# Performance work log

Hardware: AMD Instinct MI355X
Metric: run time of the kernel (lower is better)

## Reference

```python
import jax, jax.numpy as jnp
import numpy as np

H = 1024
B = 8
S = 2048

def setup_inputs() -> dict:
    key = jax.random.key(0)
    ks = jax.random.split(key, 16)
    w = lambda k, shp: (jax.random.normal(k, shp, dtype=jnp.float32) * 0.02)
    return {
        "hidden_states": jax.random.normal(ks[0], (B, S, H), dtype=jnp.float32),
        "context_vector": jax.random.normal(ks[1], (B, H), dtype=jnp.float32),
        # nn.Linear weights stored torch-style as [out, in]
        "Wq": w(ks[2], (H, H)), "bq": w(ks[3], (H,)),
        "Wk": w(ks[4], (H, H)), "bk": w(ks[5], (H,)),
        "Wv": w(ks[6], (H, H)), "bv": w(ks[7], (H,)),
        "Wcq": w(ks[8], (H, H)),  # only .weight.t() used in original (no bias)
        "Wck": w(ks[9], (H, H)),
        "g_qh": jax.random.normal(ks[10], (H, 1), dtype=jnp.float32),
        "g_kh": jax.random.normal(ks[11], (H, 1), dtype=jnp.float32),
        "g_qc": jax.random.normal(ks[12], (H, 1), dtype=jnp.float32),
        "g_kc": jax.random.normal(ks[13], (H, 1), dtype=jnp.float32),
    }

def reference(hidden_states, context_vector, Wq, bq, Wk, bk, Wv, bv, Wcq, Wck, g_qh, g_kh, g_qc, g_kc):
    # Linear projections (torch Linear: x @ W.T + b)
    query = jnp.einsum('bsh,oh->bso', hidden_states, Wq) + bq   # [B,S,H]
    key_  = jnp.einsum('bsh,oh->bso', hidden_states, Wk) + bk
    value = jnp.einsum('bsh,oh->bso', hidden_states, Wv) + bv

    # gate = sigmoid(Q @ g_h + (ctx @ g_c)[:,None,:])  -> [B,S,1]
    q_gate = jax.nn.sigmoid(query @ g_qh + (context_vector @ g_qc)[:, None, :])
    k_gate = jax.nn.sigmoid(key_  @ g_kh + (context_vector @ g_kc)[:, None, :])

    # context projections: ctx @ weight.t() (no bias in original usage) -> [B,1,H]
    ctx_q = (context_vector @ Wcq.T)[:, None, :]
    ctx_k = (context_vector @ Wck.T)[:, None, :]

    query_hat = (1.0 - q_gate) * query + q_gate * ctx_q
    key_hat   = (1.0 - k_gate) * key_  + k_gate * ctx_k

    scale = 1.0 / jnp.sqrt(jnp.asarray(H, dtype=jnp.float32))
    scores = jnp.einsum('bqh,bkh->bqk', query_hat, key_hat) * scale  # [B,S,S]
    probs = jax.nn.softmax(scores, axis=-1)
    output = jnp.einsum('bqk,bkh->bqh', probs, value)  # [B,S,H]
    return (output, scores)
```

## Files before the change

### kernel.cpp

```cpp
#include <hip/hip_runtime.h>
#include <cstdint>
#include <cstddef>

#define H 1024
#define NB 8
#define S 2048
#define MROWS (NB*S)

using short8 = __attribute__((ext_vector_type(8))) short;
using f32x4  = __attribute__((ext_vector_type(4))) float;

__device__ __forceinline__ unsigned short f2bf(float f){
  union { float f; unsigned int u; } c; c.f = f;
  unsigned int u = c.u;
  return (unsigned short)((u + 0x7fffu + ((u >> 16) & 1u)) >> 16);
}


__global__ void k_cvt3(const float* __restrict__ a, const float* __restrict__ b, const float* __restrict__ c,
                       unsigned short* __restrict__ oa, unsigned short* __restrict__ ob, unsigned short* __restrict__ oc){
  const float* src = blockIdx.y == 0 ? a : (blockIdx.y == 1 ? b : c);
  unsigned short* dst = blockIdx.y == 0 ? oa : (blockIdx.y == 1 ? ob : oc);
  int i = (blockIdx.x * 256 + threadIdx.x) * 4;
  float4 v = *reinterpret_cast<const float4*>(src + i);
  ushort4 o;
  o.x = f2bf(v.x); o.y = f2bf(v.y); o.z = f2bf(v.z); o.w = f2bf(v.w);
  *reinterpret_cast<ushort4*>(dst + i) = o;
}

__global__ void k_colproj(const float* __restrict__ Wq_, const float* __restrict__ gq_,
                          const float* __restrict__ Wk_, const float* __restrict__ gk_,
                          float* __restrict__ up){
  const float* W = blockIdx.z ? Wk_ : Wq_;
  const float* g = blockIdx.z ? gk_ : gq_;
  const int in = blockIdx.x * 256 + threadIdx.x;
  const int o0 = blockIdx.y * 128;
  float s = 0.f;
  for (int o = 0; o < 128; ++o) s = fmaf(W[(size_t)(o0 + o) * H + in], g[o0 + o], s);
  up[(blockIdx.z * 8 + blockIdx.y) * 1024 + in] = s;
}

__global__ void k_ucombine(const float* __restrict__ up, float* __restrict__ uq, float* __restrict__ uk){
  int i = blockIdx.x * 256 + threadIdx.x;
  int m = i >> 10, j = i & 1023;
  float s = 0.f;
  #pragma unroll
  for (int c = 0; c < 8; ++c) s += up[(m * 8 + c) * 1024 + j];
  (m ? uk : uq)[j] = s;
}

__global__ __launch_bounds__(256) void k_ctxproj(const float* __restrict__ Wcq, const float* __restrict__ Wck,
    const float* __restrict__ ctx, float* __restrict__ outq, float* __restrict__ outk){
  __shared__ float cs[NB * H];
  const float* W = blockIdx.y ? Wck : Wcq;
  float* out = blockIdx.y ? outk : outq;
  const int t = threadIdx.x;
  for (int i = t; i < NB * H; i += 256) cs[i] = ctx[i];
  __syncthreads();
  const int wid = t >> 6, lane = t & 63;
  const int row = blockIdx.x * 4 + wid;
  float a[NB];
  #pragma unroll
  for (int b = 0; b < NB; ++b) a[b] = 0.f;
  for (int i0 = 0; i0 < H; i0 += 64){
    const float w = W[(size_t)row * H + i0 + lane];
    #pragma unroll
    for (int b = 0; b < NB; ++b) a[b] = fmaf(w, cs[b * H + i0 + lane], a[b]);
  }
  #pragma unroll
  for (int b = 0; b < NB; ++b){
    float v = a[b];
    #pragma unroll
    for (int off = 32; off > 0; off >>= 1) v += __shfl_xor(v, off);
    if (lane == 0) out[b * H + row] = v;
  }
}

__device__ float block_dot(const float* a, const float* b, float* red, int t){
  float s = 0.f;
  for (int i = t; i < H; i += 256) s = fmaf(a[i], b[i], s);
  red[t] = s;
  __syncthreads();
  for (int off = 128; off > 0; off >>= 1){
    if (t < off) red[t] += red[t + off];
    __syncthreads();
  }
  float r = red[0];
  __syncthreads();
  return r;
}

__global__ void k_scalars(const float* __restrict__ bq, const float* __restrict__ gqh,
                          const float* __restrict__ bk, const float* __restrict__ gkh,
                          const float* __restrict__ ctx, const float* __restrict__ gqc,
                          const float* __restrict__ gkc, float* __restrict__ scal){
  __shared__ float red[256];
  const int t = threadIdx.x;
  float v;
  v = block_dot(bq, gqh, red, t); if (t == 0) scal[0] = v;
  v = block_dot(bk, gkh, red, t); if (t == 0) scal[1] = v;
  for (int b = 0; b < NB; ++b){
    v = block_dot(ctx + b * H, gqc, red, t); if (t == 0) scal[2 + b] = v;
    v = block_dot(ctx + b * H, gkc, red, t); if (t == 0) scal[10 + b] = v;
  }
}

__global__ __launch_bounds__(256) void k_prepass(const float* __restrict__ hs,
    const float* __restrict__ u_q, const float* __restrict__ u_k, const float* __restrict__ scal,
    unsigned short* __restrict__ hsb, float* __restrict__ gq, float* __restrict__ gk){
  const int t = threadIdx.x, wid = t >> 6, lane = t & 63;
  const int row = blockIdx.x * 4 + wid;
  const float* hrow = hs + (size_t)row * H;
  unsigned short* orow = hsb + (size_t)row * H;
  float sq = 0.f, sk = 0.f;
  #pragma unroll
  for (int c = 0; c < 4; ++c){
    const int idx = (lane + c * 64) * 4;
    float4 v  = *reinterpret_cast<const float4*>(hrow + idx);
    float4 uq = *reinterpret_cast<const float4*>(u_q + idx);
    float4 uk = *reinterpret_cast<const float4*>(u_k + idx);
    ushort4 o; o.x = f2bf(v.x); o.y = f2bf(v.y); o.z = f2bf(v.z); o.w = f2bf(v.w);
    *reinterpret_cast<ushort4*>(orow + idx) = o;
    sq += v.x*uq.x + v.y*uq.y + v.z*uq.z + v.w*uq.w;
    sk += v.x*uk.x + v.y*uk.y + v.z*uk.z + v.w*uk.w;
  }
  #pragma unroll
  for (int off = 32; off > 0; off >>= 1){
    sq += __shfl_xor(sq, off);
    sk += __shfl_xor(sk, off);
  }
  if (lane == 0){
    const int b = row >> 11;
    gq[row] = 1.f / (1.f + __expf(-(sq + scal[0] + scal[2 + b])));
    gk[row] = 1.f / (1.f + __expf(-(sk + scal[1] + scal[10 + b])));
  }
}


#define STG(bufi, opi, halfi, koff, P0, P1) \
  { __builtin_amdgcn_global_load_lds((const __attribute__((address_space(1))) void*)(P0 + (koff)), \
      (__attribute__((address_space(3))) void*)((char*)(&lds[bufi][opi][halfi][0]) + (wid*2+0)*1024), 16, 0, 0); \
    __builtin_amdgcn_global_load_lds((const __attribute__((address_space(1))) void*)(P1 + (koff)), \
      (__attribute__((address_space(3))) void*)((char*)(&lds[bufi][opi][halfi][0]) + (wid*2+1)*1024), 16, 0, 0); }
#define STG_A(bufi, halfi, koff) STG(bufi, 0, halfi, koff, sA0, sA1)
#define STG_B(bufi, halfi, koff) STG(bufi, 1, halfi, koff, sB0, sB1)

#define DS_A(bufi, ks, mh) \
  { _Pragma("unroll") for (int m_ = 0; m_ < 4; ++m_){ \
      const int ar_ = wr*128 + ((mh)*4 + m_)*16 + (lane & 15); \
      const int sl_ = (lane >> 4) ^ ((ar_ >> 1) & 3); \
      af[m_] = *reinterpret_cast<const short8*>(&lds[bufi][0][ks][ar_*32 + sl_*8]); } }
#define DS_B(bufi, ks) \
  { _Pragma("unroll") for (int n_ = 0; n_ < 4; ++n_){ \
      const int br_ = wc*64 + n_*16 + (lane & 15); \
      const int sl_ = (lane >> 4) ^ ((br_ >> 1) & 3); \
      bf[n_] = *reinterpret_cast<const short8*>(&lds[bufi][1][ks][br_*32 + sl_*8]); } }
#define MFMA16(mh) \
  { __builtin_amdgcn_s_setprio(1); \
    _Pragma("unroll") for (int m_ = 0; m_ < 4; ++m_) \
      _Pragma("unroll") for (int n_ = 0; n_ < 4; ++n_) \
        acc[(mh)*4 + m_][n_] = __builtin_amdgcn_mfma_f32_16x16x32_bf16(af[m_], bf[n_], acc[(mh)*4 + m_][n_], 0, 0, 0); \
    __builtin_amdgcn_s_setprio(0); }
#define VM4() asm volatile("s_waitcnt vmcnt(4)" ::: "memory");
#define VM0() asm volatile("s_waitcnt vmcnt(0)" ::: "memory");
#define BAR() { asm volatile("" ::: "memory"); __builtin_amdgcn_s_barrier(); asm volatile("" ::: "memory"); }

template<int MODE>
__global__ __launch_bounds__(512, 2)
void k_gemm(const unsigned short* __restrict__ A, const unsigned short* __restrict__ B,
            int K, int ldA, int ldB, long long Abatch, long long Bbatch,
            const float* __restrict__ gate, const float* __restrict__ bias,
            const float* __restrict__ ctxv,
            unsigned short* __restrict__ outb, float* __restrict__ outf,
            long long outBatch, float scale)
{
  __shared__ __align__(16) short lds[2][2][2][8192];

  const int t = threadIdx.x;
  const int wid = t >> 6, lane = t & 63;
  const int wr = wid >> 2, wc = wid & 3;
  const int bz = blockIdx.z;
  const unsigned short* Ab = A + (size_t)bz * (size_t)Abatch;
  const unsigned short* Bb = B + (size_t)bz * (size_t)Bbatch;
  const int row0 = blockIdx.x * 256;
  const int col0 = blockIdx.y * 256;

  const int c0 = (wid*2 + 0)*64 + lane;
  const int c1 = (wid*2 + 1)*64 + lane;
  const int r0s = c0 >> 2, r1s = c1 >> 2;
  const int kc0 = (c0 & 3) ^ ((r0s >> 1) & 3);
  const int kc1 = (c1 & 3) ^ ((r1s >> 1) & 3);
  const unsigned short* sA0 = Ab + (size_t)(row0 + r0s) * (size_t)ldA + kc0*8;
  const unsigned short* sA1 = Ab + (size_t)(row0 + r1s) * (size_t)ldA + kc1*8;
  const unsigned short* sB0 = Bb + (size_t)(col0 + r0s) * (size_t)ldB + kc0*8;
  const unsigned short* sB1 = Bb + (size_t)(col0 + r1s) * (size_t)ldB + kc1*8;

  f32x4 acc[8][4] = {};
  short8 af[4], bf[4];

  STG_A(0, 0, 0); STG_B(0, 0, 0); STG_A(0, 1, 32); STG_B(0, 1, 32);
  VM0(); BAR();

  const int niter = K >> 7;
  for (int it = 0; it < niter; ++it){
    const int t1k = (it*2 + 1) << 6;
    const int t2k = (it*2 + 2) << 6;
    const bool more = (it + 1 < niter);
    DS_A(0, 0, 0); DS_B(0, 0); STG_A(1, 0, t1k); MFMA16(0); BAR();
    DS_A(0, 0, 1); STG_B(1, 0, t1k); MFMA16(1); VM4(); BAR();
    DS_A(0, 1, 0); DS_B(0, 1); STG_A(1, 1, t1k + 32); MFMA16(0); BAR();
    DS_A(0, 1, 1); STG_B(1, 1, t1k + 32); MFMA16(1);
    if (more) { VM4(); } else { VM0(); }
    BAR();
    DS_A(1, 0, 0); DS_B(1, 0); if (more) STG_A(0, 0, t2k); MFMA16(0); BAR();
    DS_A(1, 0, 1); if (more) { STG_B(0, 0, t2k); } MFMA16(1); if (more) VM4(); BAR();
    DS_A(1, 1, 0); DS_B(1, 1); if (more) STG_A(0, 1, t2k + 32); MFMA16(0); BAR();
    DS_A(1, 1, 1); if (more) { STG_B(0, 1, t2k + 32); } MFMA16(1); if (more) VM4(); BAR();
  }

  if constexpr (MODE == 0 || MODE == 1){
    const int b = row0 >> 11;
    #pragma unroll
    for (int mi = 0; mi < 8; ++mi)
      #pragma unroll
      for (int n = 0; n < 4; ++n)
        #pragma unroll
        for (int r = 0; r < 4; ++r){
          const int grow = row0 + wr*128 + mi*16 + (lane >> 4)*4 + r;
          const int gcol = col0 + wc*64 + n*16 + (lane & 15);
          const float g = gate[grow];
          const float q = acc[mi][n][r] + bias[gcol];
          outb[(size_t)grow * H + gcol] = f2bf((1.f - g) * q + g * ctxv[b * H + gcol]);
        }
  } else if constexpr (MODE == 2){
    short* tp = (short*)lds;
    const int bb = row0 >> 11;
    const int s0 = row0 & (S - 1);
    #pragma unroll
    for (int ci = 0; ci < 2; ++ci)
      #pragma unroll
      for (int cj = 0; cj < 2; ++cj){
        __syncthreads();
        if (wr == ci && (wc >> 1) == cj){
          const int lc0 = (wc & 1) * 64;
          #pragma unroll
          for (int mi = 0; mi < 8; ++mi)
            #pragma unroll
            for (int n = 0; n < 4; ++n)
              #pragma unroll
              for (int r = 0; r < 4; ++r){
                const int lr = mi*16 + (lane >> 4)*4 + r;
                const int lc = lc0 + n*16 + (lane & 15);
                tp[lr*129 + lc] = (short)f2bf(acc[mi][n][r] + bias[col0 + cj*128 + lc]);
              }
        }
        __syncthreads();
        const int hl = t >> 2;
        const int sb = (t & 3) * 32;
        unsigned short* vout = outb + (size_t)bb * H * S + (size_t)(col0 + cj*128 + hl) * S
                                    + (size_t)(s0 + ci*128 + sb);
        #pragma unroll
        for (int i2 = 0; i2 < 32; i2 += 4){
          ushort4 o;
          o.x = (unsigned short)tp[(sb + i2 + 0)*129 + hl];
          o.y = (unsigned short)tp[(sb + i2 + 1)*129 + hl];
          o.z = (unsigned short)tp[(sb + i2 + 2)*129 + hl];
          o.w = (unsigned short)tp[(sb + i2 + 3)*129 + hl];
          *reinterpret_cast<ushort4*>(vout + i2) = o;
        }
      }
  } else if constexpr (MODE == 3){
    #pragma unroll
    for (int mi = 0; mi < 8; ++mi)
      #pragma unroll
      for (int n = 0; n < 4; ++n)
        #pragma unroll
        for (int r = 0; r < 4; ++r){
          const int grow = row0 + wr*128 + mi*16 + (lane >> 4)*4 + r;
          const int gcol = col0 + wc*64 + n*16 + (lane & 15);
          outf[(size_t)bz * (size_t)outBatch + (size_t)grow * S + gcol] = acc[mi][n][r] * scale;
        }
  } else {
    #pragma unroll
    for (int mi = 0; mi < 8; ++mi)
      #pragma unroll
      for (int n = 0; n < 4; ++n)
        #pragma unroll
        for (int r = 0; r < 4; ++r){
          const int grow = row0 + wr*128 + mi*16 + (lane >> 4)*4 + r;
          const int gcol = col0 + wc*64 + n*16 + (lane & 15);
          outf[(size_t)bz * (size_t)outBatch + (size_t)grow * H + gcol] = acc[mi][n][r];
        }
  }
}

__global__ __launch_bounds__(256) void k_softmax(const float* __restrict__ scores,
                                                 unsigned short* __restrict__ probs){
  const int row = blockIdx.x;
  const float* srow = scores + (size_t)row * S;
  unsigned short* prow = probs + (size_t)row * S;
  const int t = threadIdx.x, wid = t >> 6, lane = t & 63;
  __shared__ float red[8];
  float4 v0 = *reinterpret_cast<const float4*>(srow + t * 4);
  float4 v1 = *reinterpret_cast<const float4*>(srow + 1024 + t * 4);
  float m = fmaxf(fmaxf(fmaxf(v0.x, v0.y), fmaxf(v0.z, v0.w)),
                  fmaxf(fmaxf(v1.x, v1.y), fmaxf(v1.z, v1.w)));
  #pragma unroll
  for (int off = 32; off > 0; off >>= 1) m = fmaxf(m, __shfl_xor(m, off));
  if (lane == 0) red[wid] = m;
  __syncthreads();
  m = fmaxf(fmaxf(red[0], red[1]), fmaxf(red[2], red[3]));
  float4 e0, e1;
  e0.x = __expf(v0.x - m); e0.y = __expf(v0.y - m); e0.z = __expf(v0.z - m); e0.w = __expf(v0.w - m);
  e1.x = __expf(v1.x - m); e1.y = __expf(v1.y - m); e1.z = __expf(v1.z - m); e1.w = __expf(v1.w - m);
  float s = (e0.x + e0.y + e0.z + e0.w) + (e1.x + e1.y + e1.z + e1.w);
  #pragma unroll
  for (int off = 32; off > 0; off >>= 1) s += __shfl_xor(s, off);
  if (lane == 0) red[4 + wid] = s;
  __syncthreads();
  s = (red[4] + red[5]) + (red[6] + red[7]);
  const float inv = 1.f / s;
  ushort4 o;
  o.x = f2bf(e0.x * inv); o.y = f2bf(e0.y * inv); o.z = f2bf(e0.z * inv); o.w = f2bf(e0.w * inv);
  *reinterpret_cast<ushort4*>(prow + t * 4) = o;
  o.x = f2bf(e1.x * inv); o.y = f2bf(e1.y * inv); o.z = f2bf(e1.z * inv); o.w = f2bf(e1.w * inv);
  *reinterpret_cast<ushort4*>(prow + 1024 + t * 4) = o;
}

extern "C" void kernel_launch(void* const* d_in, const int* in_sizes, int n_in,
                              void* d_out, int out_size, void* d_ws, size_t ws_size,
                              hipStream_t stream) {
  const float* hs  = (const float*)d_in[0];
  const float* ctx = (const float*)d_in[1];
  const float* Wq  = (const float*)d_in[2];
  const float* bq  = (const float*)d_in[3];
  const float* Wk  = (const float*)d_in[4];
  const float* bk  = (const float*)d_in[5];
  const float* Wv  = (const float*)d_in[6];
  const float* bv  = (const float*)d_in[7];
  const float* Wcq = (const float*)d_in[8];
  const float* Wck = (const float*)d_in[9];
  const float* gqh = (const float*)d_in[10];
  const float* gkh = (const float*)d_in[11];
  const float* gqc = (const float*)d_in[12];
  const float* gkc = (const float*)d_in[13];

  char* ws = (char*)d_ws;
  const size_t T = (size_t)MROWS * H * 2;
  unsigned short* hsb  = (unsigned short*)(ws);
  unsigned short* qhat = (unsigned short*)(ws + T);
  unsigned short* khat = (unsigned short*)(ws + 2 * T);
  unsigned short* vt   = (unsigned short*)(ws + 3 * T);
  unsigned short* wqb  = (unsigned short*)(ws + 4 * T);
  unsigned short* wkb  = (unsigned short*)(ws + 4 * T + 2097152);
  unsigned short* wvb  = (unsigned short*)(ws + 4 * T + 4194304);
  float* fb    = (float*)(ws + 4 * T + 6291456);
  float* u_q   = fb;
  float* u_k   = fb + 1024;
  float* ctxq  = fb + 2048;
  float* ctxk  = fb + 10240;
  float* gq    = fb + 18432;
  float* gk    = fb + 34816;
  float* scal  = fb + 51200;
  float* u_part= fb + 51232;
  unsigned short* probs = (unsigned short*)ws;

  float* out_attn   = (float*)d_out;
  float* out_scores = out_attn + (size_t)MROWS * H;

  k_cvt3<<<dim3(1024, 3), 256, 0, stream>>>(Wq, Wk, Wv, wqb, wkb, wvb);
  k_colproj<<<dim3(4, 8, 2), 256, 0, stream>>>(Wq, gqh, Wk, gkh, u_part);
  k_ucombine<<<8, 256, 0, stream>>>(u_part, u_q, u_k);
  k_ctxproj<<<dim3(256, 2), 256, 0, stream>>>(Wcq, Wck, ctx, ctxq, ctxk);
  k_scalars<<<1, 256, 0, stream>>>(bq, gqh, bk, gkh, ctx, gqc, gkc, scal);
  k_prepass<<<MROWS / 4, 256, 0, stream>>>(hs, u_q, u_k, scal, hsb, gq, gk);

  k_gemm<0><<<dim3(64, 4, 1), 512, 0, stream>>>(hsb, wqb, 1024, 1024, 1024, 0, 0,
      gq, bq, ctxq, qhat, nullptr, 0, 1.f);
  k_gemm<1><<<dim3(64, 4, 1), 512, 0, stream>>>(hsb, wkb, 1024, 1024, 1024, 0, 0,
      gk, bk, ctxk, khat, nullptr, 0, 1.f);
  k_gemm<2><<<dim3(64, 4, 1), 512, 0, stream>>>(hsb, wvb, 1024, 1024, 1024, 0, 0,
      nullptr, bv, nullptr, vt, nullptr, 0, 1.f);

  k_gemm<3><<<dim3(8, 8, 8), 512, 0, stream>>>(qhat, khat, 1024, 1024, 1024,
      (long long)S * H, (long long)S * H, nullptr, nullptr, nullptr,
      nullptr, out_scores, (long long)S * S, 0.03125f);

  k_softmax<<<MROWS, 256, 0, stream>>>(out_scores, probs);

  k_gemm<4><<<dim3(8, 4, 8), 512, 0, stream>>>(probs, vt, 2048, 2048, 2048,
      (long long)S * S, (long long)H * S, nullptr, nullptr, nullptr,
      nullptr, out_attn, (long long)S * H, 1.f);
}
```

Measured before the change: 357.0 us.

## Restage GEMM epilogues through LDS, add explicit waits in mainloop, parallelize scalars

The Q/K projection epilogue now stages gated bf16 results in LDS and writes them out with 16-byte vector stores, replacing scattered 2-byte global writes. The V-transpose epilogue uses a column-major LDS tile so it can emit 8-wide vector stores. The GEMM main loop gains an extra barrier plus an lgkmcnt(0) wait with a sched_barrier before each MFMA block, which enforces ordering but may reduce overlap of LDS reads with compute. Separately, k_scalars switches to a one-wave-per-dot-product shuffle reduction, and the workspace layout is changed so probs no longer aliases hsb.

```diff
diff --git a/kernel.cpp b/kernel.cpp
--- a/kernel.cpp
+++ b/kernel.cpp
@@ -7,8 +7,9 @@
 #define S 2048
 #define MROWS (NB*S)
 
-using short8 = __attribute__((ext_vector_type(8))) short;
-using f32x4  = __attribute__((ext_vector_type(4))) float;
+using short8  = __attribute__((ext_vector_type(8))) short;
+using ushort8 = __attribute__((ext_vector_type(8))) unsigned short;
+using f32x4   = __attribute__((ext_vector_type(4))) float;
 
 __device__ __forceinline__ unsigned short f2bf(float f){
   union { float f; unsigned int u; } c; c.f = f;
@@ -28,25 +29,26 @@
   *reinterpret_cast<ushort4*>(dst + i) = o;
 }
 
-__global__ void k_colproj(const float* __restrict__ Wq_, const float* __restrict__ gq_,
-                          const float* __restrict__ Wk_, const float* __restrict__ gk_,
+__global__ void k_colproj(const float* __restrict__ Wq_, const float* __restrict__ Wk_,
+                          const float* __restrict__ gqh, const float* __restrict__ gkh,
                           float* __restrict__ up){
-  const float* W = blockIdx.z ? Wk_ : Wq_;
-  const float* g = blockIdx.z ? gk_ : gq_;
+  const int z = blockIdx.z;
+  const float* W = z ? Wk_ : Wq_;
+  const float* g = z ? gkh : gqh;
   const int in = blockIdx.x * 256 + threadIdx.x;
   const int o0 = blockIdx.y * 128;
   float s = 0.f;
   for (int o = 0; o < 128; ++o) s = fmaf(W[(size_t)(o0 + o) * H + in], g[o0 + o], s);
-  up[(blockIdx.z * 8 + blockIdx.y) * 1024 + in] = s;
-}
-
-__global__ void k_ucombine(const float* __restrict__ up, float* __restrict__ uq, float* __restrict__ uk){
+  up[(z * 8 + blockIdx.y) * 1024 + in] = s;
+}
+
+__global__ void k_ucombine(const float* __restrict__ up, float* __restrict__ u2){
   int i = blockIdx.x * 256 + threadIdx.x;
-  int m = i >> 10, j = i & 1023;
+  int z = i >> 10, h = i & 1023;
   float s = 0.f;
   #pragma unroll
-  for (int c = 0; c < 8; ++c) s += up[(m * 8 + c) * 1024 + j];
-  (m ? uk : uq)[j] = s;
+  for (int c = 0; c < 8; ++c) s += up[(z * 8 + c) * 1024 + h];
+  u2[i] = s;
 }
 
 __global__ __launch_bounds__(256) void k_ctxproj(const float* __restrict__ Wcq, const float* __restrict__ Wck,
@@ -76,41 +78,33 @@
   }
 }
 
-__device__ float block_dot(const float* a, const float* b, float* red, int t){
-  float s = 0.f;
-  for (int i = t; i < H; i += 256) s = fmaf(a[i], b[i], s);
-  red[t] = s;
-  __syncthreads();
-  for (int off = 128; off > 0; off >>= 1){
-    if (t < off) red[t] += red[t + off];
-    __syncthreads();
-  }
-  float r = red[0];
-  __syncthreads();
-  return r;
-}
-
-__global__ void k_scalars(const float* __restrict__ bq, const float* __restrict__ gqh,
-                          const float* __restrict__ bk, const float* __restrict__ gkh,
-                          const float* __restrict__ ctx, const float* __restrict__ gqc,
-                          const float* __restrict__ gkc, float* __restrict__ scal){
-  __shared__ float red[256];
-  const int t = threadIdx.x;
-  float v;
-  v = block_dot(bq, gqh, red, t); if (t == 0) scal[0] = v;
-  v = block_dot(bk, gkh, red, t); if (t == 0) scal[1] = v;
-  for (int b = 0; b < NB; ++b){
-    v = block_dot(ctx + b * H, gqc, red, t); if (t == 0) scal[2 + b] = v;
-    v = block_dot(ctx + b * H, gkc, red, t); if (t == 0) scal[10 + b] = v;
+__global__ __launch_bounds__(512) void k_scalars(const float* __restrict__ bq, const float* __restrict__ gqh,
+    const float* __restrict__ bk, const float* __restrict__ gkh,
+    const float* __restrict__ ctx, const float* __restrict__ gqc, const float* __restrict__ gkc,
+    float* __restrict__ scal){
+  const int wid = threadIdx.x >> 6, lane = threadIdx.x & 63;
+  for (int d = wid; d < 18; d += 8){
+    const float *pa, *pb;
+    if (d == 0){ pa = bq; pb = gqh; }
+    else if (d == 1){ pa = bk; pb = gkh; }
+    else if (d < 10){ pa = ctx + (d - 2) * H; pb = gqc; }
+    else { pa = ctx + (d - 10) * H; pb = gkc; }
+    float s = 0.f;
+    for (int i = lane; i < H; i += 64) s = fmaf(pa[i], pb[i], s);
+    #pragma unroll
+    for (int off = 32; off > 0; off >>= 1) s += __shfl_xor(s, off);
+    if (lane == 0) scal[d] = s;
   }
 }
 
 __global__ __launch_bounds__(256) void k_prepass(const float* __restrict__ hs,
-    const float* __restrict__ u_q, const float* __restrict__ u_k, const float* __restrict__ scal,
+    const float* __restrict__ u2, const float* __restrict__ scal,
     unsigned short* __restrict__ hsb, float* __restrict__ gq, float* __restrict__ gk){
   const int t = threadIdx.x, wid = t >> 6, lane = t & 63;
   const int row = blockIdx.x * 4 + wid;
   const float* hrow = hs + (size_t)row * H;
+  const float* u_q = u2;
+  const float* u_k = u2 + 1024;
   unsigned short* orow = hsb + (size_t)row * H;
   float sq = 0.f, sk = 0.f;
   #pragma unroll
@@ -138,32 +132,33 @@
 
 
 #define STG(bufi, opi, halfi, koff, P0, P1) \
-  { __builtin_amdgcn_global_load_lds((const __attribute__((address_space(1))) void*)(P0 + (koff)), \
+  do { __builtin_amdgcn_global_load_lds((const __attribute__((address_space(1))) void*)(P0 + (koff)), \
       (__attribute__((address_space(3))) void*)((char*)(&lds[bufi][opi][halfi][0]) + (wid*2+0)*1024), 16, 0, 0); \
     __builtin_amdgcn_global_load_lds((const __attribute__((address_space(1))) void*)(P1 + (koff)), \
-      (__attribute__((address_space(3))) void*)((char*)(&lds[bufi][opi][halfi][0]) + (wid*2+1)*1024), 16, 0, 0); }
+      (__attribute__((address_space(3))) void*)((char*)(&lds[bufi][opi][halfi][0]) + (wid*2+1)*1024), 16, 0, 0); } while(0)
 #define STG_A(bufi, halfi, koff) STG(bufi, 0, halfi, koff, sA0, sA1)
 #define STG_B(bufi, halfi, koff) STG(bufi, 1, halfi, koff, sB0, sB1)
 
 #define DS_A(bufi, ks, mh) \
-  { _Pragma("unroll") for (int m_ = 0; m_ < 4; ++m_){ \
+  do { _Pragma("unroll") for (int m_ = 0; m_ < 4; ++m_){ \
       const int ar_ = wr*128 + ((mh)*4 + m_)*16 + (lane & 15); \
       const int sl_ = (lane >> 4) ^ ((ar_ >> 1) & 3); \
-      af[m_] = *reinterpret_cast<const short8*>(&lds[bufi][0][ks][ar_*32 + sl_*8]); } }
+      af[m_] = *reinterpret_cast<const short8*>(&lds[bufi][0][ks][ar_*32 + sl_*8]); } } while(0)
 #define DS_B(bufi, ks) \
-  { _Pragma("unroll") for (int n_ = 0; n_ < 4; ++n_){ \
+  do { _Pragma("unroll") for (int n_ = 0; n_ < 4; ++n_){ \
       const int br_ = wc*64 + n_*16 + (lane & 15); \
       const int sl_ = (lane >> 4) ^ ((br_ >> 1) & 3); \
-      bf[n_] = *reinterpret_cast<const short8*>(&lds[bufi][1][ks][br_*32 + sl_*8]); } }
+      bf[n_] = *reinterpret_cast<const short8*>(&lds[bufi][1][ks][br_*32 + sl_*8]); } } while(0)
 #define MFMA16(mh) \
-  { __builtin_amdgcn_s_setprio(1); \
+  do { __builtin_amdgcn_s_setprio(1); \
     _Pragma("unroll") for (int m_ = 0; m_ < 4; ++m_) \
       _Pragma("unroll") for (int n_ = 0; n_ < 4; ++n_) \
         acc[(mh)*4 + m_][n_] = __builtin_amdgcn_mfma_f32_16x16x32_bf16(af[m_], bf[n_], acc[(mh)*4 + m_][n_], 0, 0, 0); \
-    __builtin_amdgcn_s_setprio(0); }
-#define VM4() asm volatile("s_waitcnt vmcnt(4)" ::: "memory");
-#define VM0() asm volatile("s_waitcnt vmcnt(0)" ::: "memory");
-#define BAR() { asm volatile("" ::: "memory"); __builtin_amdgcn_s_barrier(); asm volatile("" ::: "memory"); }
+    __builtin_amdgcn_s_setprio(0); } while(0)
+#define VM4() do { asm volatile("s_waitcnt vmcnt(4)" ::: "memory"); } while(0)
+#define VM0() do { asm volatile("s_waitcnt vmcnt(0)" ::: "memory"); } while(0)
+#define BAR() do { asm volatile("" ::: "memory"); __builtin_amdgcn_s_barrier(); asm volatile("" ::: "memory"); } while(0)
+#define LGKM0() do { asm volatile("s_waitcnt lgkmcnt(0)" ::: "memory"); __builtin_amdgcn_sched_barrier(0); } while(0)
 
 template<int MODE>
 __global__ __launch_bounds__(512, 2)
@@ -206,34 +201,58 @@
     const int t1k = (it*2 + 1) << 6;
     const int t2k = (it*2 + 2) << 6;
     const bool more = (it + 1 < niter);
-    DS_A(0, 0, 0); DS_B(0, 0); STG_A(1, 0, t1k); MFMA16(0); BAR();
-    DS_A(0, 0, 1); STG_B(1, 0, t1k); MFMA16(1); VM4(); BAR();
-    DS_A(0, 1, 0); DS_B(0, 1); STG_A(1, 1, t1k + 32); MFMA16(0); BAR();
-    DS_A(0, 1, 1); STG_B(1, 1, t1k + 32); MFMA16(1);
-    if (more) { VM4(); } else { VM0(); }
-    BAR();
-    DS_A(1, 0, 0); DS_B(1, 0); if (more) STG_A(0, 0, t2k); MFMA16(0); BAR();
-    DS_A(1, 0, 1); if (more) { STG_B(0, 0, t2k); } MFMA16(1); if (more) VM4(); BAR();
-    DS_A(1, 1, 0); DS_B(1, 1); if (more) STG_A(0, 1, t2k + 32); MFMA16(0); BAR();
-    DS_A(1, 1, 1); if (more) { STG_B(0, 1, t2k + 32); } MFMA16(1); if (more) VM4(); BAR();
-  }
-
-  if constexpr (MODE == 0 || MODE == 1){
+    DS_A(0, 0, 0); DS_B(0, 0); STG_A(1, 0, t1k);      BAR(); LGKM0(); MFMA16(0);                              BAR();
+    DS_A(0, 0, 1);             STG_B(1, 0, t1k);      BAR(); LGKM0(); MFMA16(1); VM4();                       BAR();
+    DS_A(0, 1, 0); DS_B(0, 1); STG_A(1, 1, t1k + 32); BAR(); LGKM0(); MFMA16(0);                              BAR();
+    DS_A(0, 1, 1);             STG_B(1, 1, t1k + 32); BAR(); LGKM0(); MFMA16(1); if (more) { VM4(); } else { VM0(); } BAR();
+    DS_A(1, 0, 0); DS_B(1, 0); if (more) { STG_A(0, 0, t2k); }      BAR(); LGKM0(); MFMA16(0);                BAR();
+    DS_A(1, 0, 1);             if (more) { STG_B(0, 0, t2k); }      BAR(); LGKM0(); MFMA16(1); if (more) { VM4(); } BAR();
+    DS_A(1, 1, 0); DS_B(1, 1); if (more) { STG_A(0, 1, t2k + 32); } BAR(); LGKM0(); MFMA16(0);                BAR();
+    DS_A(1, 1, 1);             if (more) { STG_B(0, 1, t2k + 32); } BAR(); LGKM0(); MFMA16(1); if (more) { VM4(); } BAR();
+  }
+
+  if constexpr (MODE == 0){
+    unsigned short* tp = (unsigned short*)lds;
+    float* gl = (float*)((char*)lds + 69632);
+    float* bl = gl + 256;
+    float* cl = bl + 256;
     const int b = row0 >> 11;
-    #pragma unroll
-    for (int mi = 0; mi < 8; ++mi)
+    __syncthreads();
+    if (t < 256){
+      gl[t] = gate[row0 + t];
+      bl[t] = bias[col0 + t];
+      cl[t] = ctxv[b * H + col0 + t];
+    }
+    __syncthreads();
+    #pragma unroll
+    for (int ci = 0; ci < 2; ++ci){
+      if (ci) __syncthreads();
+      if (wr == ci){
+        #pragma unroll
+        for (int mi = 0; mi < 8; ++mi)
+          #pragma unroll
+          for (int r = 0; r < 4; ++r){
+            const int lr = mi*16 + (lane >> 4)*4 + r;
+            const float g = gl[ci*128 + lr];
+            #pragma unroll
+            for (int n = 0; n < 4; ++n){
+              const int lc = wc*64 + n*16 + (lane & 15);
+              const float q = acc[mi][n][r] + bl[lc];
+              tp[lr*264 + lc] = f2bf((1.f - g) * q + g * cl[lc]);
+            }
+          }
+      }
+      __syncthreads();
+      const int rr = t & 127;
+      const int cc = (t >> 7) * 64;
+      const unsigned short* srcp = tp + rr*264 + cc;
+      unsigned short* dst = outb + (size_t)(row0 + ci*128 + rr) * H + col0 + cc;
       #pragma unroll
-      for (int n = 0; n < 4; ++n)
-        #pragma unroll
-        for (int r = 0; r < 4; ++r){
-          const int grow = row0 + wr*128 + mi*16 + (lane >> 4)*4 + r;
-          const int gcol = col0 + wc*64 + n*16 + (lane & 15);
-          const float g = gate[grow];
-          const float q = acc[mi][n][r] + bias[gcol];
-          outb[(size_t)grow * H + gcol] = f2bf((1.f - g) * q + g * ctxv[b * H + gcol]);
-        }
+      for (int i = 0; i < 64; i += 8)
+        *reinterpret_cast<ushort8*>(dst + i) = *reinterpret_cast<const ushort8*>(srcp + i);
+    }
   } else if constexpr (MODE == 2){
-    short* tp = (short*)lds;
+    unsigned short* tp = (unsigned short*)lds;
     const int bb = row0 >> 11;
     const int s0 = row0 & (S - 1);
     #pragma unroll
@@ -251,23 +270,18 @@
               for (int r = 0; r < 4; ++r){
                 const int lr = mi*16 + (lane >> 4)*4 + r;
                 const int lc = lc0 + n*16 + (lane & 15);
-                tp[lr*129 + lc] = (short)f2bf(acc[mi][n][r] + bias[col0 + cj*128 + lc]);
+                tp[lc*136 + lr] = f2bf(acc[mi][n][r] + bias[col0 + cj*128 + lc]);
               }
         }
         __syncthreads();
-        const int hl = t >> 2;
-        const int sb = (t & 3) * 32;
-        unsigned short* vout = outb + (size_t)bb * H * S + (size_t)(col0 + cj*128 + hl) * S
-                                    + (size_t)(s0 + ci*128 + sb);
+        const int hh = t & 127;
+        const int sc = (t >> 7) * 32;
+        const unsigned short* srcp = tp + hh*136 + sc;
+        unsigned short* vout = outb + (size_t)bb * H * S + (size_t)(col0 + cj*128 + hh) * S
+                                    + (size_t)(s0 + ci*128 + sc);
         #pragma unroll
-        for (int i2 = 0; i2 < 32; i2 += 4){
-          ushort4 o;
-          o.x = (unsigned short)tp[(sb + i2 + 0)*129 + hl];
-          o.y = (unsigned short)tp[(sb + i2 + 1)*129 + hl];
-          o.z = (unsigned short)tp[(sb + i2 + 2)*129 + hl];
-          o.w = (unsigned short)tp[(sb + i2 + 3)*129 + hl];
-          *reinterpret_cast<ushort4*>(vout + i2) = o;
-        }
+        for (int i2 = 0; i2 < 32; i2 += 8)
+          *reinterpret_cast<ushort8*>(vout + i2) = *reinterpret_cast<const ushort8*>(srcp + i2);
       }
   } else if constexpr (MODE == 3){
     #pragma unroll
@@ -346,39 +360,37 @@
   const float* gkc = (const float*)d_in[13];
 
   char* ws = (char*)d_ws;
-  const size_t T = (size_t)MROWS * H * 2;
-  unsigned short* hsb  = (unsigned short*)(ws);
-  unsigned short* qhat = (unsigned short*)(ws + T);
-  unsigned short* khat = (unsigned short*)(ws + 2 * T);
-  unsigned short* vt   = (unsigned short*)(ws + 3 * T);
-  unsigned short* wqb  = (unsigned short*)(ws + 4 * T);
-  unsigned short* wkb  = (unsigned short*)(ws + 4 * T + 2097152);
-  unsigned short* wvb  = (unsigned short*)(ws + 4 * T + 4194304);
-  float* fb    = (float*)(ws + 4 * T + 6291456);
-  float* u_q   = fb;
-  float* u_k   = fb + 1024;
-  float* ctxq  = fb + 2048;
-  float* ctxk  = fb + 10240;
-  float* gq    = fb + 18432;
-  float* gk    = fb + 34816;
-  float* scal  = fb + 51200;
-  float* u_part= fb + 51232;
-  unsigned short* probs = (unsigned short*)ws;
+  unsigned short* hsb   = (unsigned short*)(ws);
+  unsigned short* qhat  = (unsigned short*)(ws + 33554432);
+  unsigned short* khat  = (unsigned short*)(ws + 67108864);
+  unsigned short* vt    = (unsigned short*)(ws + 100663296);
+  unsigned short* probs = (unsigned short*)(ws + 134217728);
+  unsigned short* wqb   = (unsigned short*)(ws + 167772160);
+  unsigned short* wkb   = (unsigned short*)(ws + 169869312);
+  unsigned short* wvb   = (unsigned short*)(ws + 171966464);
+  float* up    = (float*)(ws + 174063616);
+  float* u2    = (float*)(ws + 174129152);
+  float* ctxq  = (float*)(ws + 174137344);
+  float* ctxk  = (float*)(ws + 174170112);
+  float* gq    = (float*)(ws + 174202880);
+  float* gk    = (float*)(ws + 174268416);
+  float* scal  = (float*)(ws + 174333952);
 
   float* out_attn   = (float*)d_out;
   float* out_scores = out_attn + (size_t)MROWS * H;
 
   k_cvt3<<<dim3(1024, 3), 256, 0, stream>>>(Wq, Wk, Wv, wqb, wkb, wvb);
-  k_colproj<<<dim3(4, 8, 2), 256, 0, stream>>>(Wq, gqh, Wk, gkh, u_part);
-  k_ucombine<<<8, 256, 0, stream>>>(u_part, u_q, u_k);
+  k_colproj<<<dim3(4, 8, 2), 256, 0, stream>>>(Wq, Wk, gqh, gkh, up);
+  k_ucombine<<<8, 256, 0, stream>>>(up, u2);
   k_ctxproj<<<dim3(256, 2), 256, 0, stream>>>(Wcq, Wck, ctx, ctxq, ctxk);
-  k_scalars<<<1, 256, 0, stream>>>(bq, gqh, bk, gkh, ctx, gqc, gkc, scal);
-  k_prepass<<<MROWS / 4, 256, 0, stream>>>(hs, u_q, u_k, scal, hsb, gq, gk);
+  k_scalars<<<1, 512, 0, stream>>>(bq, gqh, bk, gkh, ctx, gqc, gkc, scal);
+  k_prepass<<<MROWS / 4, 256, 0, stream>>>(hs, u2, scal, hsb, gq, gk);
 
   k_gemm<0><<<dim3(64, 4, 1), 512, 0, stream>>>(hsb, wqb, 1024, 1024, 1024, 0, 0,
       gq, bq, ctxq, qhat, nullptr, 0, 1.f);
-  k_gemm<1><<<dim3(64, 4, 1), 512, 0, stream>>>(hsb, wkb, 1024, 1024, 1024, 0, 0,
+  k_gemm<0><<<dim3(64, 4, 1), 512, 0, stream>>>(hsb, wkb, 1024, 1024, 1024, 0, 0,
       gk, bk, ctxk, khat, nullptr, 0, 1.f);
+
   k_gemm<2><<<dim3(64, 4, 1), 512, 0, stream>>>(hsb, wvb, 1024, 1024, 1024, 0, 0,
       nullptr, bv, nullptr, vt, nullptr, 0, 1.f);
 
```

New measurement: 369.7 us. +3.6%, slower.
